# Kernel tuning notes

Hardware: AMD Instinct MI355X
Metric: run time of the kernel (lower is better)

The kernel has to match this reference:

```python
import jax, jax.numpy as jnp
import numpy as np

BASE_SCALE = 60.0
EPS = 1e-8


def _nearest_D8(x):
    """Nearest point in D8 lattice (integer vectors with even coordinate sum), x: [..., 8]."""
    f = jnp.round(x)
    d = x - f
    parity_even = (jnp.mod(jnp.sum(f, axis=-1), 2.0) == 0.0)
    # flip rounding at the coordinate with the largest rounding error
    idx = jnp.argmax(jnp.abs(d), axis=-1)
    delta = jnp.where(d >= 0, 1.0, -1.0).astype(x.dtype)
    onehot = jax.nn.one_hot(idx, 8, dtype=x.dtype)
    flip = jnp.take_along_axis(delta, idx[..., None], axis=-1)
    g = f + onehot * flip
    return jnp.where(parity_even[..., None], f, g)


def _e8_quantize(x):
    """Nearest point in E8 = D8 U (D8 + 1/2), x: [..., 8]."""
    y0 = _nearest_D8(x)
    y1 = _nearest_D8(x - 0.5) + 0.5
    d0 = jnp.sum((x - y0) ** 2, axis=-1, keepdims=True)
    d1 = jnp.sum((x - y1) ** 2, axis=-1, keepdims=True)
    return jnp.where(d0 <= d1, y0, y1)


def _quantize_with_row_scaling(w):
    """Row-norm scale -> E8 lattice quantize on 8-dim blocks -> rescale back."""
    n_rows = w.shape[0]
    adaptive = min(2.0, max(0.5, n_rows / 10000.0))
    sf = jnp.asarray(BASE_SCALE * adaptive, dtype=w.dtype)
    row_norms = jnp.linalg.norm(w, axis=1, keepdims=True)  # [out, 1]
    row_norms_safe = jnp.maximum(row_norms, EPS)
    w_scaled = (w / row_norms_safe) * sf
    q = _e8_quantize(w_scaled.reshape(-1, 8)).reshape(w.shape)
    return q * row_norms_safe / sf


def setup_inputs() -> dict:
    key = jax.random.key(0)
    k1, k2, k3 = jax.random.split(key, 3)
    B, IN, OUT = 4096, 4096, 4096
    x = jax.random.normal(k1, (B, IN), dtype=jnp.float32)
    weight = jax.random.normal(k2, (OUT, IN), dtype=jnp.float32) * 0.1
    bias = jax.random.normal(k3, (OUT,), dtype=jnp.float32)
    return {"x": x, "weight": weight, "bias": bias}


def reference(x, weight, bias):
    wq = _quantize_with_row_scaling(weight)
    return x @ wq.T + bias
```

## Files before the change

### kernel.cpp

```cpp
#include <hip/hip_runtime.h>
#include <hip/hip_bf16.h>

typedef __bf16 bf16_t;
typedef __bf16 bf16x8 __attribute__((ext_vector_type(8)));
typedef float f32x4 __attribute__((ext_vector_type(4)));

#define GLL16(gp, lp)                                                          \
    __builtin_amdgcn_global_load_lds(                                          \
        (const __attribute__((address_space(1))) void*)(gp),                   \
        (__attribute__((address_space(3))) void*)(lp), 16, 0, 0)

#define SBAR() __builtin_amdgcn_s_barrier()
#define SCHED0() __builtin_amdgcn_sched_barrier(0)
#define WAIT_VM8() asm volatile("s_waitcnt vmcnt(8)" ::: "memory")
#define WAIT_VM0() asm volatile("s_waitcnt vmcnt(0)" ::: "memory")
#define MFMA_(d, a, b)                                                         \
    d = __builtin_amdgcn_mfma_f32_16x16x32_bf16(a, b, d, 0, 0, 0)


__device__ __forceinline__ void nearest_D8_d(const double x[8], double f[8]) {
    double d[8];
    double fs = 0.0;
#pragma unroll
    for (int i = 0; i < 8; ++i) {
        f[i] = rint(x[i]);
        d[i] = x[i] - f[i];
        fs += f[i];
    }
    long long s = (long long)fs;
    if (s & 1LL) {
        int idx = 0;
        double best = fabs(d[0]);
#pragma unroll
        for (int i = 1; i < 8; ++i) {
            double a = fabs(d[i]);
            if (a > best) { best = a; idx = i; }
        }
        f[idx] += (d[idx] >= 0.0) ? 1.0 : -1.0;
    }
}

__device__ __forceinline__ void e8_quantize_d(const double x[8], float q[8]) {
    double y0[8], y1[8], xs[8];
    nearest_D8_d(x, y0);
#pragma unroll
    for (int i = 0; i < 8; ++i) xs[i] = x[i] - 0.5;
    nearest_D8_d(xs, y1);
#pragma unroll
    for (int i = 0; i < 8; ++i) y1[i] += 0.5;
    double d0 = 0.0, d1 = 0.0;
#pragma unroll
    for (int i = 0; i < 8; ++i) {
        double a = x[i] - y0[i]; d0 += a * a;
        double b = x[i] - y1[i]; d1 += b * b;
    }
    bool take0 = (d0 <= d1);
#pragma unroll
    for (int i = 0; i < 8; ++i) q[i] = (float)(take0 ? y0[i] : y1[i]);
}

__global__ __launch_bounds__(256) void prep_kernel(
    const float* __restrict__ W, bf16_t* __restrict__ Q,
    float* __restrict__ scale, int IN, double sfd,
    const float* __restrict__ x, bf16_t* __restrict__ Xb, long long n8,
    int OUT, int CB)
{
    if (blockIdx.x >= (unsigned)OUT) {
        long long i = (long long)(blockIdx.x - OUT) * 256 + threadIdx.x;
        long long stride = (long long)CB * 256;
        for (; i < n8; i += stride) {
            float4 v0 = *(const float4*)(x + i * 8);
            float4 v1 = *(const float4*)(x + i * 8 + 4);
            bf16x8 o;
            o[0] = (bf16_t)v0.x; o[1] = (bf16_t)v0.y;
            o[2] = (bf16_t)v0.z; o[3] = (bf16_t)v0.w;
            o[4] = (bf16_t)v1.x; o[5] = (bf16_t)v1.y;
            o[6] = (bf16_t)v1.z; o[7] = (bf16_t)v1.w;
            *(bf16x8*)(Xb + i * 8) = o;
        }
        return;
    }
    const int row  = blockIdx.x;
    const int t    = threadIdx.x;
    const int lane = t & 63, w = t >> 6;
    const float* wrow = W + (size_t)row * IN;

    double ss = 0.0;
    for (int i = t; i < (IN >> 2); i += 256) {
        float4 v = *(const float4*)(wrow + i * 4);
        double a = v.x, b = v.y, c = v.z, d = v.w;
        ss += a * a + b * b + c * c + d * d;
    }
#pragma unroll
    for (int m = 1; m < 64; m <<= 1) ss += __shfl_xor(ss, m);
    __shared__ double red[4];
    if (lane == 0) red[w] = ss;
    __syncthreads();
    double S   = (red[0] + red[1]) + (red[2] + red[3]);
    double nsd = fmax(sqrt(S), 1e-8);

    for (int b = t; b < (IN >> 3); b += 256) {
        const float* xp = wrow + b * 8;
        float4 v0 = *(const float4*)xp;
        float4 v1 = *(const float4*)(xp + 4);
        double xd[8] = {v0.x, v0.y, v0.z, v0.w, v1.x, v1.y, v1.z, v1.w};
        double xsd[8];
#pragma unroll
        for (int i = 0; i < 8; ++i) xsd[i] = (xd[i] / nsd) * sfd;
        float qf[8];
        e8_quantize_d(xsd, qf);
        bf16x8 o;
#pragma unroll
        for (int i = 0; i < 8; ++i) o[i] = (bf16_t)qf[i];
        *(bf16x8*)(Q + (size_t)row * IN + b * 8) = o;
    }
    if (t == 0) scale[row] = (float)(nsd / sfd);
}


#define BM 256
#define BN 256
#define BK 64

__global__ __launch_bounds__(512, 2) void gemm_kernel(
    const bf16_t* __restrict__ A,
    const bf16_t* __restrict__ B,
    const float* __restrict__ scale,
    const float* __restrict__ bias,
    float* __restrict__ C,
    int M, int N, int K)
{
    __shared__ __align__(16) bf16_t lds[2][2][2][8192];

    const int t    = threadIdx.x;
    const int lane = t & 63;
    const int w    = t >> 6;
    const int wr   = w >> 2;
    const int wc   = w & 3;

    const int nwg = gridDim.x;
    const int bid = blockIdx.x;
    const int q8 = nwg >> 3, r8 = nwg & 7;
    const int xcd = bid & 7, idx = bid >> 3;
    const int swz = (xcd < r8 ? xcd * (q8 + 1) : r8 * (q8 + 1) + (xcd - r8) * q8) + idx;
    const int nbx = N / BN;
    const int bx = swz % nbx, by = swz / nbx;

    const int rowq  = t >> 3;
    const int kslot = ((t & 7) ^ (rowq & 7)) << 3;
    const bf16_t* gA = A + (size_t)(by * BM + rowq) * K + kslot;
    const bf16_t* gB = B + (size_t)(bx * BN + rowq) * K + kslot;

#define STAGE(isB, bufi, h, kt)                                                \
    do {                                                                       \
        const bf16_t* s_ = ((isB) ? gB : gA)                                   \
            + (size_t)(h) * 128 * (size_t)K + (size_t)(kt) * BK;               \
        GLL16(s_,                   &lds[bufi][isB][h][t * 8]);                \
        GLL16(s_ + 64 * (size_t)K,  &lds[bufi][isB][h][t * 8 + 4096]);         \
    } while (0)

    const int l15  = lane & 15;
    const int koff = lane >> 4;
    const int aoff0 = l15 * 64 + (((koff)     ^ (lane & 7)) << 3);
    const int aoff1 = l15 * 64 + (((4 + koff) ^ (lane & 7)) << 3);

    f32x4 acc[8][4];
    const f32x4 zero = {0.f, 0.f, 0.f, 0.f};
#pragma unroll
    for (int R = 0; R < 8; ++R)
#pragma unroll
        for (int Cf = 0; Cf < 4; ++Cf) acc[R][Cf] = zero;

    const int NT = K / BK;

    STAGE(1, 0, 0, 0); STAGE(1, 0, 1, 0);
    STAGE(0, 0, 0, 0); STAGE(0, 0, 1, 0);
    if (NT > 1) {
        STAGE(1, 1, 0, 1); STAGE(1, 1, 1, 1);
        STAGE(0, 1, 0, 1); STAGE(0, 1, 1, 1);
        WAIT_VM8();
    } else {
        WAIT_VM0();
    }
    SBAR();
    SCHED0();

    bf16x8 af[4][2], b01[2][2], b23[2][2];

    for (int kt = 0; kt < NT; ++kt) {
        const int cur = kt & 1;
        const bf16_t* ldsA = &lds[cur][0][wr][0];
        const bf16_t* ldsB = &lds[cur][1][wc >> 1][(wc & 1) * 4096];
        const bool s2 = (kt + 2 < NT);

#pragma unroll
        for (int R = 0; R < 4; ++R) {
            af[R][0] = *(const bf16x8*)(ldsA + R * 1024 + aoff0);
            af[R][1] = *(const bf16x8*)(ldsA + R * 1024 + aoff1);
        }
#pragma unroll
        for (int c = 0; c < 2; ++c) {
            b01[c][0] = *(const bf16x8*)(ldsB + c * 1024 + aoff0);
            b01[c][1] = *(const bf16x8*)(ldsB + c * 1024 + aoff1);
        }
#pragma unroll
        for (int c = 0; c < 2; ++c) {
            b23[c][0] = *(const bf16x8*)(ldsB + (2 + c) * 1024 + aoff0);
            b23[c][1] = *(const bf16x8*)(ldsB + (2 + c) * 1024 + aoff1);
        }
        __builtin_amdgcn_s_setprio(1);
#pragma unroll
        for (int s = 0; s < 2; ++s)
#pragma unroll
            for (int R = 0; R < 4; ++R) {
                MFMA_(acc[R][0], af[R][s], b01[0][s]);
                MFMA_(acc[R][1], af[R][s], b01[1][s]);
            }
#pragma unroll
        for (int s = 0; s < 2; ++s)
#pragma unroll
            for (int R = 0; R < 4; ++R) {
                MFMA_(acc[R][2], af[R][s], b23[0][s]);
                MFMA_(acc[R][3], af[R][s], b23[1][s]);
            }
        __builtin_amdgcn_s_setprio(0);
        SBAR();
        SCHED0();

#pragma unroll
        for (int R = 0; R < 4; ++R) {
            af[R][0] = *(const bf16x8*)(ldsA + (4 + R) * 1024 + aoff0);
            af[R][1] = *(const bf16x8*)(ldsA + (4 + R) * 1024 + aoff1);
        }
        if (s2) { STAGE(1, cur, 0, kt + 2); STAGE(1, cur, 1, kt + 2); }
        __builtin_amdgcn_s_setprio(1);
#pragma unroll
        for (int s = 0; s < 2; ++s)
#pragma unroll
            for (int R = 0; R < 4; ++R) {
                MFMA_(acc[4 + R][2], af[R][s], b23[0][s]);
                MFMA_(acc[4 + R][3], af[R][s], b23[1][s]);
            }
        __builtin_amdgcn_s_setprio(0);
        SBAR();
        SCHED0();

        if (s2) { STAGE(0, cur, 0, kt + 2); STAGE(0, cur, 1, kt + 2); }
        __builtin_amdgcn_s_setprio(1);
#pragma unroll
        for (int s = 0; s < 2; ++s)
#pragma unroll
            for (int R = 0; R < 4; ++R) {
                MFMA_(acc[4 + R][0], af[R][s], b01[0][s]);
                MFMA_(acc[4 + R][1], af[R][s], b01[1][s]);
            }
        __builtin_amdgcn_s_setprio(0);
        if (kt < NT - 2) { WAIT_VM8(); }
        else if (kt == NT - 2) { WAIT_VM0(); }
        SBAR();
        SCHED0();
    }

    const int r0 = by * BM + wr * 128 + (lane >> 4) * 4;
    const int c0 = bx * BN + wc * 64 + l15;
#pragma unroll
    for (int Cf = 0; Cf < 4; ++Cf) {
        const int col = c0 + Cf * 16;
        const float sc = scale[col];
        const float bi = bias[col];
#pragma unroll
        for (int R = 0; R < 8; ++R) {
            const int row = r0 + R * 16;
#pragma unroll
            for (int j = 0; j < 4; ++j)
                C[(size_t)(row + j) * N + col] = acc[R][Cf][j] * sc + bi;
        }
    }
#undef STAGE
}


extern "C" void kernel_launch(void* const* d_in, const int* in_sizes, int n_in,
                              void* d_out, int out_size, void* d_ws, size_t ws_size,
                              hipStream_t stream)
{
    const float* x    = (const float*)d_in[0];
    const float* wgt  = (const float*)d_in[1];
    const float* bias = (const float*)d_in[2];

    const int OUT = in_sizes[2];
    const int IN  = (int)((long long)in_sizes[1] / OUT);
    const int M   = (int)((long long)in_sizes[0] / IN);
    const int N = OUT, K = IN;

    double ad = (double)OUT / 10000.0;
    if (ad < 0.5) ad = 0.5;
    if (ad > 2.0) ad = 2.0;
    const double sfd = 60.0 * ad;

    bf16_t* Q  = (bf16_t*)d_ws;
    bf16_t* Xb = (bf16_t*)((char*)d_ws + (size_t)OUT * IN * sizeof(bf16_t));
    float*  sc = (float*)((char*)d_ws + (size_t)OUT * IN * sizeof(bf16_t)
                                      + (size_t)M * IN * sizeof(bf16_t));
    float*  C  = (float*)d_out;

    long long n8 = (long long)M * IN / 8;
    const int CB = 2048;
    prep_kernel<<<OUT + CB, 256, 0, stream>>>(wgt, Q, sc, IN, sfd,
                                              x, Xb, n8, OUT, CB);

    int grid = (M / BM) * (N / BN);
    gemm_kernel<<<grid, 512, 0, stream>>>(Xb, Q, sc, bias, C, M, N, K);
}
```

Before: 157.8 us.

## Prefetch next K-tile LDS fragments across iterations and merge global staging

Restructures the GEMM main loop so that each k-half's A/B fragments come from LDS one phase ahead. The next tile's first-half fragments are loaded during the current tile's second-half MFMAs, which overlaps LDS reads with matrix math. All four global-to-LDS stages for tile kt+2 are now issued together after one barrier, and the loop needs one fewer barrier per iteration. This raises register pressure (full 8x A and 4x B fragment arrays for two halves) and drops the NT==1 guard in the prologue.

```diff
diff --git a/kernel.cpp b/kernel.cpp
--- a/kernel.cpp
+++ b/kernel.cpp
@@ -14,6 +14,7 @@
 #define SCHED0() __builtin_amdgcn_sched_barrier(0)
 #define WAIT_VM8() asm volatile("s_waitcnt vmcnt(8)" ::: "memory")
 #define WAIT_VM0() asm volatile("s_waitcnt vmcnt(0)" ::: "memory")
+#define WAIT_LGKM0() asm volatile("s_waitcnt lgkmcnt(0)" ::: "memory")
 #define MFMA_(d, a, b)                                                         \
     d = __builtin_amdgcn_mfma_f32_16x16x32_bf16(a, b, d, 0, 0, 0)
 
@@ -175,90 +176,82 @@
 
     STAGE(1, 0, 0, 0); STAGE(1, 0, 1, 0);
     STAGE(0, 0, 0, 0); STAGE(0, 0, 1, 0);
-    if (NT > 1) {
-        STAGE(1, 1, 0, 1); STAGE(1, 1, 1, 1);
-        STAGE(0, 1, 0, 1); STAGE(0, 1, 1, 1);
-        WAIT_VM8();
-    } else {
-        WAIT_VM0();
-    }
+    STAGE(1, 1, 0, 1); STAGE(1, 1, 1, 1);
+    STAGE(0, 1, 0, 1); STAGE(0, 1, 1, 1);
+    WAIT_VM8();
     SBAR();
     SCHED0();
 
-    bf16x8 af[4][2], b01[2][2], b23[2][2];
+    bf16x8 fA0[8], fA1[8], fB0[4], fB1[4];
+
+    {
+        const bf16_t* ldsA0 = &lds[0][0][wr][0];
+        const bf16_t* ldsB0 = &lds[0][1][wc >> 1][(wc & 1) * 4096];
+#pragma unroll
+        for (int R = 0; R < 8; ++R)
+            fA0[R] = *(const bf16x8*)(ldsA0 + R * 1024 + aoff0);
+#pragma unroll
+        for (int c = 0; c < 4; ++c)
+            fB0[c] = *(const bf16x8*)(ldsB0 + c * 1024 + aoff0);
+    }
 
     for (int kt = 0; kt < NT; ++kt) {
         const int cur = kt & 1;
-        const bf16_t* ldsA = &lds[cur][0][wr][0];
-        const bf16_t* ldsB = &lds[cur][1][wc >> 1][(wc & 1) * 4096];
-        const bool s2 = (kt + 2 < NT);
-
-#pragma unroll
-        for (int R = 0; R < 4; ++R) {
-            af[R][0] = *(const bf16x8*)(ldsA + R * 1024 + aoff0);
-            af[R][1] = *(const bf16x8*)(ldsA + R * 1024 + aoff1);
-        }
-#pragma unroll
-        for (int c = 0; c < 2; ++c) {
-            b01[c][0] = *(const bf16x8*)(ldsB + c * 1024 + aoff0);
-            b01[c][1] = *(const bf16x8*)(ldsB + c * 1024 + aoff1);
-        }
-#pragma unroll
-        for (int c = 0; c < 2; ++c) {
-            b23[c][0] = *(const bf16x8*)(ldsB + (2 + c) * 1024 + aoff0);
-            b23[c][1] = *(const bf16x8*)(ldsB + (2 + c) * 1024 + aoff1);
-        }
+        const bf16_t* ldsAc = &lds[cur][0][wr][0];
+        const bf16_t* ldsBc = &lds[cur][1][wc >> 1][(wc & 1) * 4096];
+        const bf16_t* ldsAn = &lds[cur ^ 1][0][wr][0];
+        const bf16_t* ldsBn = &lds[cur ^ 1][1][wc >> 1][(wc & 1) * 4096];
+
+#pragma unroll
+        for (int R = 0; R < 8; ++R)
+            fA1[R] = *(const bf16x8*)(ldsAc + R * 1024 + aoff1);
+#pragma unroll
+        for (int c = 0; c < 4; ++c)
+            fB1[c] = *(const bf16x8*)(ldsBc + c * 1024 + aoff1);
         __builtin_amdgcn_s_setprio(1);
 #pragma unroll
-        for (int s = 0; s < 2; ++s)
-#pragma unroll
-            for (int R = 0; R < 4; ++R) {
-                MFMA_(acc[R][0], af[R][s], b01[0][s]);
-                MFMA_(acc[R][1], af[R][s], b01[1][s]);
-            }
-#pragma unroll
-        for (int s = 0; s < 2; ++s)
-#pragma unroll
-            for (int R = 0; R < 4; ++R) {
-                MFMA_(acc[R][2], af[R][s], b23[0][s]);
-                MFMA_(acc[R][3], af[R][s], b23[1][s]);
-            }
+        for (int R = 0; R < 8; ++R)
+#pragma unroll
+            for (int c = 0; c < 4; ++c)
+                MFMA_(acc[R][c], fA0[R], fB0[c]);
         __builtin_amdgcn_s_setprio(0);
+        SCHED0();
+        WAIT_LGKM0();
         SBAR();
         SCHED0();
 
-#pragma unroll
-        for (int R = 0; R < 4; ++R) {
-            af[R][0] = *(const bf16x8*)(ldsA + (4 + R) * 1024 + aoff0);
-            af[R][1] = *(const bf16x8*)(ldsA + (4 + R) * 1024 + aoff1);
-        }
-        if (s2) { STAGE(1, cur, 0, kt + 2); STAGE(1, cur, 1, kt + 2); }
+        if (kt + 2 < NT) {
+            STAGE(1, cur, 0, kt + 2); STAGE(1, cur, 1, kt + 2);
+            STAGE(0, cur, 0, kt + 2); STAGE(0, cur, 1, kt + 2);
+        }
         __builtin_amdgcn_s_setprio(1);
 #pragma unroll
-        for (int s = 0; s < 2; ++s)
-#pragma unroll
-            for (int R = 0; R < 4; ++R) {
-                MFMA_(acc[4 + R][2], af[R][s], b23[0][s]);
-                MFMA_(acc[4 + R][3], af[R][s], b23[1][s]);
-            }
+        for (int R = 0; R < 8; ++R) {
+            MFMA_(acc[R][0], fA1[R], fB1[0]);
+            MFMA_(acc[R][1], fA1[R], fB1[1]);
+        }
         __builtin_amdgcn_s_setprio(0);
-        SBAR();
         SCHED0();
-
-        if (s2) { STAGE(0, cur, 0, kt + 2); STAGE(0, cur, 1, kt + 2); }
-        __builtin_amdgcn_s_setprio(1);
-#pragma unroll
-        for (int s = 0; s < 2; ++s)
-#pragma unroll
-            for (int R = 0; R < 4; ++R) {
-                MFMA_(acc[4 + R][0], af[R][s], b01[0][s]);
-                MFMA_(acc[4 + R][1], af[R][s], b01[1][s]);
-            }
-        __builtin_amdgcn_s_setprio(0);
         if (kt < NT - 2) { WAIT_VM8(); }
         else if (kt == NT - 2) { WAIT_VM0(); }
         SBAR();
         SCHED0();
+
+        if (kt + 1 < NT) {
+#pragma unroll
+            for (int R = 0; R < 8; ++R)
+                fA0[R] = *(const bf16x8*)(ldsAn + R * 1024 + aoff0);
+#pragma unroll
+            for (int c = 0; c < 4; ++c)
+                fB0[c] = *(const bf16x8*)(ldsBn + c * 1024 + aoff0);
+        }
+        __builtin_amdgcn_s_setprio(1);
+#pragma unroll
+        for (int R = 0; R < 8; ++R) {
+            MFMA_(acc[R][2], fA1[R], fB1[2]);
+            MFMA_(acc[R][3], fA1[R], fB1[3]);
+        }
+        __builtin_amdgcn_s_setprio(0);
     }
 
     const int r0 = by * BM + wr * 128 + (lane >> 4) * 4;
```

New measurement: 158.2 us. Within noise of the previous version (+0.3%).

## Fuse fp32-to-bf16 activation conversion into GEMM A-tile loading

Applied to the files above, without the earlier changes.

Removes the separate x-to-bf16 conversion pass from the prep kernel. The GEMM now loads fp32 activations into registers, converts them to bf16 and writes them to LDS itself, with the loads issued two tiles ahead. This avoids writing and rereading a 32 MB bf16 copy of x. In exchange, A traffic per tile doubles because each block reads fp32, and every block that shares a row tile redoes the conversion. The fetch also moves from direct global-to-LDS loads to register staging, which adds VGPR pressure and changes the vmcnt wait logic.

```diff
diff --git a/kernel.cpp b/kernel.cpp
--- a/kernel.cpp
+++ b/kernel.cpp
@@ -12,8 +12,10 @@
 
 #define SBAR() __builtin_amdgcn_s_barrier()
 #define SCHED0() __builtin_amdgcn_sched_barrier(0)
-#define WAIT_VM8() asm volatile("s_waitcnt vmcnt(8)" ::: "memory")
+#define WAIT_VM16() asm volatile("s_waitcnt vmcnt(16)" ::: "memory")
+#define WAIT_VM4() asm volatile("s_waitcnt vmcnt(4)" ::: "memory")
 #define WAIT_VM0() asm volatile("s_waitcnt vmcnt(0)" ::: "memory")
+#define WAIT_LGKM0() asm volatile("s_waitcnt lgkmcnt(0)" ::: "memory")
 #define MFMA_(d, a, b)                                                         \
     d = __builtin_amdgcn_mfma_f32_16x16x32_bf16(a, b, d, 0, 0, 0)
 
@@ -59,27 +61,10 @@
     for (int i = 0; i < 8; ++i) q[i] = (float)(take0 ? y0[i] : y1[i]);
 }
 
-__global__ __launch_bounds__(256) void prep_kernel(
+__global__ __launch_bounds__(256) void quant_kernel(
     const float* __restrict__ W, bf16_t* __restrict__ Q,
-    float* __restrict__ scale, int IN, double sfd,
-    const float* __restrict__ x, bf16_t* __restrict__ Xb, long long n8,
-    int OUT, int CB)
+    float* __restrict__ scale, int IN, double sfd)
 {
-    if (blockIdx.x >= (unsigned)OUT) {
-        long long i = (long long)(blockIdx.x - OUT) * 256 + threadIdx.x;
-        long long stride = (long long)CB * 256;
-        for (; i < n8; i += stride) {
-            float4 v0 = *(const float4*)(x + i * 8);
-            float4 v1 = *(const float4*)(x + i * 8 + 4);
-            bf16x8 o;
-            o[0] = (bf16_t)v0.x; o[1] = (bf16_t)v0.y;
-            o[2] = (bf16_t)v0.z; o[3] = (bf16_t)v0.w;
-            o[4] = (bf16_t)v1.x; o[5] = (bf16_t)v1.y;
-            o[6] = (bf16_t)v1.z; o[7] = (bf16_t)v1.w;
-            *(bf16x8*)(Xb + i * 8) = o;
-        }
-        return;
-    }
     const int row  = blockIdx.x;
     const int t    = threadIdx.x;
     const int lane = t & 63, w = t >> 6;
@@ -123,7 +108,7 @@
 #define BK 64
 
 __global__ __launch_bounds__(512, 2) void gemm_kernel(
-    const bf16_t* __restrict__ A,
+    const float* __restrict__ X,
     const bf16_t* __restrict__ B,
     const float* __restrict__ scale,
     const float* __restrict__ bias,
@@ -148,15 +133,46 @@
 
     const int rowq  = t >> 3;
     const int kslot = ((t & 7) ^ (rowq & 7)) << 3;
-    const bf16_t* gA = A + (size_t)(by * BM + rowq) * K + kslot;
+    const float*  gX = X + (size_t)(by * BM + rowq) * K + kslot;
     const bf16_t* gB = B + (size_t)(bx * BN + rowq) * K + kslot;
 
-#define STAGE(isB, bufi, h, kt)                                                \
+#define STAGEB(bufi, h, kt)                                                    \
     do {                                                                       \
-        const bf16_t* s_ = ((isB) ? gB : gA)                                   \
-            + (size_t)(h) * 128 * (size_t)K + (size_t)(kt) * BK;               \
-        GLL16(s_,                   &lds[bufi][isB][h][t * 8]);                \
-        GLL16(s_ + 64 * (size_t)K,  &lds[bufi][isB][h][t * 8 + 4096]);         \
+        const bf16_t* s_ = gB + (size_t)(h) * 128 * (size_t)K                  \
+                              + (size_t)(kt) * BK;                             \
+        GLL16(s_,                   &lds[bufi][1][h][t * 8]);                  \
+        GLL16(s_ + 64 * (size_t)K,  &lds[bufi][1][h][t * 8 + 4096]);           \
+    } while (0)
+
+#define A_LOAD(FV, kt)                                                         \
+    do {                                                                       \
+        const float* p_ = gX + (size_t)(kt) * BK;                              \
+        FV[0] = *(const f32x4*)(p_);                                           \
+        FV[1] = *(const f32x4*)(p_ + 4);                                       \
+        FV[2] = *(const f32x4*)(p_ + 64 * (size_t)K);                          \
+        FV[3] = *(const f32x4*)(p_ + 64 * (size_t)K + 4);                      \
+        FV[4] = *(const f32x4*)(p_ + 128 * (size_t)K);                         \
+        FV[5] = *(const f32x4*)(p_ + 128 * (size_t)K + 4);                     \
+        FV[6] = *(const f32x4*)(p_ + 192 * (size_t)K);                         \
+        FV[7] = *(const f32x4*)(p_ + 192 * (size_t)K + 4);                     \
+    } while (0)
+
+#define A_WRITE(FV, bufi)                                                      \
+    do {                                                                       \
+        _Pragma("unroll")                                                      \
+        for (int h_ = 0; h_ < 2; ++h_) {                                       \
+            _Pragma("unroll")                                                  \
+            for (int q_ = 0; q_ < 2; ++q_) {                                   \
+                f32x4 lo_ = FV[h_ * 4 + q_ * 2];                               \
+                f32x4 hi_ = FV[h_ * 4 + q_ * 2 + 1];                           \
+                bf16x8 v_;                                                     \
+                v_[0] = (bf16_t)lo_[0]; v_[1] = (bf16_t)lo_[1];                \
+                v_[2] = (bf16_t)lo_[2]; v_[3] = (bf16_t)lo_[3];                \
+                v_[4] = (bf16_t)hi_[0]; v_[5] = (bf16_t)hi_[1];                \
+                v_[6] = (bf16_t)hi_[2]; v_[7] = (bf16_t)hi_[3];                \
+                *(bf16x8*)(&lds[bufi][0][h_][t * 8 + q_ * 4096]) = v_;         \
+            }                                                                  \
+        }                                                                      \
     } while (0)
 
     const int l15  = lane & 15;
@@ -173,17 +189,22 @@
 
     const int NT = K / BK;
 
-    STAGE(1, 0, 0, 0); STAGE(1, 0, 1, 0);
-    STAGE(0, 0, 0, 0); STAGE(0, 0, 1, 0);
-    if (NT > 1) {
-        STAGE(1, 1, 0, 1); STAGE(1, 1, 1, 1);
-        STAGE(0, 1, 0, 1); STAGE(0, 1, 1, 1);
-        WAIT_VM8();
-    } else {
-        WAIT_VM0();
-    }
-    SBAR();
-    SCHED0();
+    f32x4 fst[8];
+
+    {
+        f32x4 f0[8], f1[8];
+        A_LOAD(f0, 0);
+        STAGEB(0, 0, 0); STAGEB(0, 1, 0);
+        A_LOAD(f1, 1);
+        STAGEB(1, 0, 1); STAGEB(1, 1, 1);
+        WAIT_VM16();
+        A_WRITE(f0, 0);
+        WAIT_VM4();
+        A_WRITE(f1, 1);
+        WAIT_LGKM0();
+        SBAR();
+        SCHED0();
+    }
 
     bf16x8 af[4][2], b01[2][2], b23[2][2];
 
@@ -193,6 +214,7 @@
         const bf16_t* ldsB = &lds[cur][1][wc >> 1][(wc & 1) * 4096];
         const bool s2 = (kt + 2 < NT);
 
+        if (s2) A_LOAD(fst, kt + 2);
 #pragma unroll
         for (int R = 0; R < 4; ++R) {
             af[R][0] = *(const bf16x8*)(ldsA + R * 1024 + aoff0);
@@ -232,7 +254,7 @@
             af[R][0] = *(const bf16x8*)(ldsA + (4 + R) * 1024 + aoff0);
             af[R][1] = *(const bf16x8*)(ldsA + (4 + R) * 1024 + aoff1);
         }
-        if (s2) { STAGE(1, cur, 0, kt + 2); STAGE(1, cur, 1, kt + 2); }
+        if (s2) { STAGEB(cur, 0, kt + 2); STAGEB(cur, 1, kt + 2); }
         __builtin_amdgcn_s_setprio(1);
 #pragma unroll
         for (int s = 0; s < 2; ++s)
@@ -245,7 +267,6 @@
         SBAR();
         SCHED0();
 
-        if (s2) { STAGE(0, cur, 0, kt + 2); STAGE(0, cur, 1, kt + 2); }
         __builtin_amdgcn_s_setprio(1);
 #pragma unroll
         for (int s = 0; s < 2; ++s)
@@ -255,8 +276,10 @@
                 MFMA_(acc[4 + R][1], af[R][s], b01[1][s]);
             }
         __builtin_amdgcn_s_setprio(0);
-        if (kt < NT - 2) { WAIT_VM8(); }
+        if (kt < NT - 2) { WAIT_VM4(); }
         else if (kt == NT - 2) { WAIT_VM0(); }
+        if (s2) A_WRITE(fst, cur);
+        WAIT_LGKM0();
         SBAR();
         SCHED0();
     }
@@ -276,7 +299,9 @@
                 C[(size_t)(row + j) * N + col] = acc[R][Cf][j] * sc + bi;
         }
     }
-#undef STAGE
+#undef STAGEB
+#undef A_LOAD
+#undef A_WRITE
 }
 
 
@@ -299,16 +324,11 @@
     const double sfd = 60.0 * ad;
 
     bf16_t* Q  = (bf16_t*)d_ws;
-    bf16_t* Xb = (bf16_t*)((char*)d_ws + (size_t)OUT * IN * sizeof(bf16_t));
-    float*  sc = (float*)((char*)d_ws + (size_t)OUT * IN * sizeof(bf16_t)
-                                      + (size_t)M * IN * sizeof(bf16_t));
+    float*  sc = (float*)((char*)d_ws + (size_t)OUT * IN * sizeof(bf16_t));
     float*  C  = (float*)d_out;
 
-    long long n8 = (long long)M * IN / 8;
-    const int CB = 2048;
-    prep_kernel<<<OUT + CB, 256, 0, stream>>>(wgt, Q, sc, IN, sfd,
-                                              x, Xb, n8, OUT, CB);
+    quant_kernel<<<OUT, 256, 0, stream>>>(wgt, Q, sc, IN, sfd);
 
     int grid = (M / BM) * (N / BN);
-    gemm_kernel<<<grid, 512, 0, stream>>>(Xb, Q, sc, bias, C, M, N, K);
-}
+    gemm_kernel<<<grid, 512, 0, stream>>>(x, Q, sc, bias, C, M, N, K);
+}
```

Result: slower. 166.6 us (+5.6%).
